# Performance work log

Hardware: AMD Instinct MI355X
Metric: run time of the kernel (lower is better)

The kernel has to match this reference:

```python
import jax, jax.numpy as jnp
import numpy as np

N = 50000      # nodes
E = 800000     # edges
F = 128        # node_features
DSS = 64       # degree_set_size
H = 128        # latent dim (hardcoded in GraphES)


def gcn_conv(x, W, b, src, dst, n):
    # PyG GCNConv: linear -> symmetric-normalized aggregation with self loops -> bias
    h = x @ W                                            # [N, C_out]
    deg = jnp.zeros((n,), x.dtype).at[dst].add(1.0) + 1.0  # in-degree incl. self loop
    dinv = jax.lax.rsqrt(deg)
    norm = dinv[src] * dinv[dst]                         # [E]
    agg = jnp.zeros_like(h).at[dst].add(h[src] * norm[:, None])
    agg = agg + h * (dinv * dinv)[:, None]               # self-loop term (norm_ii = 1/deg_i)
    return agg + b


def mlp(x, w1, b1, w2, b2):
    return jax.nn.relu(x @ w1 + b1) @ w2 + b2


def _swap(ei, i1, i2, coin):
    e1 = jnp.take(ei, i1, axis=1)
    e2 = jnp.take(ei, i2, axis=1)
    a, b = e1[0], e1[1]
    c, d = e2[0], e2[1]
    ne1 = jnp.where(coin, jnp.stack([a, d]), jnp.stack([a, c]))
    ne2 = jnp.where(coin, jnp.stack([c, b]), jnp.stack([b, d]))
    return ei.at[:, i1].set(ne1).at[:, i2].set(ne2)


def setup_inputs() -> dict:
    key = jax.random.key(0)
    ks = jax.random.split(key, 24)
    s = 0.05

    def rn(k, shape):
        return jax.random.normal(k, shape, jnp.float32) * s

    return {
        "x": jax.random.normal(ks[0], (N, F), jnp.float32),
        "edge_index": jax.random.randint(ks[1], (2, E), 0, N, dtype=jnp.int32),
        "degree_set": jax.random.randint(ks[2], (N,), 0, DSS, dtype=jnp.int32),
        "timesteps": 5,
        # encoder: GCN(F+DSS -> 2H), GCN(2H -> H)
        "enc_w1": rn(ks[3], (F + DSS, 2 * H)), "enc_b1": jnp.zeros((2 * H,), jnp.float32),
        "enc_w2": rn(ks[4], (2 * H, H)),       "enc_b2": jnp.zeros((H,), jnp.float32),
        # decoder: GCN(H+DSS -> 2F), GCN(2F -> F)
        "dec_w1": rn(ks[5], (H + DSS, 2 * F)), "dec_b1": jnp.zeros((2 * F,), jnp.float32),
        "dec_w2": rn(ks[6], (2 * F, F)),       "dec_b2": jnp.zeros((F,), jnp.float32),
        # edge_predictor_1: Linear(128,64)->ReLU->Linear(64,1)
        "ep1_w1": rn(ks[7], (H, 64)),  "ep1_b1": jnp.zeros((64,), jnp.float32),
        "ep1_w2": rn(ks[8], (64, 1)),  "ep1_b2": jnp.zeros((1,), jnp.float32),
        # edge_predictor_2: input is z concat flattened pair features -> 128+256=384
        "ep2_w1": rn(ks[9], (H + 2 * H, 64)), "ep2_b1": jnp.zeros((64,), jnp.float32),
        "ep2_w2": rn(ks[10], (64, 1)),        "ep2_b2": jnp.zeros((1,), jnp.float32),
    }


def reference(x, edge_index, degree_set, timesteps,
              enc_w1, enc_b1, enc_w2, enc_b2,
              dec_w1, dec_b1, dec_w2, dec_b2,
              ep1_w1, ep1_b1, ep1_w2, ep1_b2,
              ep2_w1, ep2_b1, ep2_w2, ep2_b2):
    src, dst = edge_index[0], edge_index[1]
    dh = jax.nn.one_hot(degree_set, DSS, dtype=x.dtype)  # [N, DSS]

    # ---- encoder ----
    h = jax.nn.relu(gcn_conv(jnp.concatenate([x, dh], 1), enc_w1, enc_b1, src, dst, N))
    z = gcn_conv(h, enc_w2, enc_b2, src, dst, N)          # [N, H]

    # ---- forward diffusion: timesteps random edge swaps (deterministic PRNG) ----
    ei = edge_index
    for t in range(timesteps):
        k1, k2 = jax.random.split(jax.random.fold_in(jax.random.key(1), t))
        idx = jax.random.choice(k1, E, (2,), replace=False)
        ei = _swap(ei, idx[0], idx[1], jax.random.bernoulli(k2))

    # ---- reverse process: argmax-driven edge swaps ----
    # edge_predictor_1 scores depend only on z -> identical every step; compute once
    i1 = jnp.argmax(mlp(z, ep1_w1, ep1_b1, ep1_w2, ep1_b2).squeeze(-1))
    for t in range(timesteps):
        e1 = jnp.take(ei, i1, axis=1)                     # [2]
        e1f = z[e1].reshape(-1)                           # [2H]
        cond = jnp.concatenate([z, jnp.broadcast_to(e1f, (N, 2 * H))], 1)
        i2 = jnp.argmax(mlp(cond, ep2_w1, ep2_b1, ep2_w2, ep2_b2).squeeze(-1))
        coin = jax.random.bernoulli(jax.random.fold_in(jax.random.key(2), t))
        ei = _swap(ei, i1, i2, coin)

    # ---- decoder on final edge structure ----
    src2, dst2 = ei[0], ei[1]
    hd = jax.nn.relu(gcn_conv(jnp.concatenate([z, dh], 1), dec_w1, dec_b1, src2, dst2, N))
    out = gcn_conv(hd, dec_w2, dec_b2, src2, dst2, N)     # [N, F]
    return out, ei
```

## Files before the change

kernel.cpp:

```cpp
#include <hip/hip_runtime.h>
#include <cstdint>
#include <cstddef>
#include <vector>
#include <algorithm>

#define NN 50000
#define EE 800000
#define FF 128
#define HH 128
#define TSTEPS 5

typedef __attribute__((ext_vector_type(8))) short bf16x8;
typedef __attribute__((ext_vector_type(4))) float f32x4;

__device__ __forceinline__ float bf2f(unsigned short u)
{
    return __uint_as_float((unsigned)u << 16);
}
__device__ __forceinline__ unsigned short f2bf(float x)
{
    unsigned u = __float_as_uint(x);
    u = (u + 0x7FFFu + ((u >> 16) & 1u));
    return (unsigned short)(u >> 16);
}
// ... 118 lines not shown
            for (int r = 0; r < 4; r++) {
                int row_in = rowBase + rt * 16 + quad * 4 + r;
                float v = acc[rt][tt][r] + bv;
                if (RELU) v = fmaxf(v, 0.f);
                Ot[row_in * BC + col_in] = f2bf(v);
            }
    }
    __syncthreads();
    for (int idx = tid; idx < 128 * (BC / 8); idx += 256) {
        int rr = idx / (BC / 8), c8 = idx - rr * (BC / 8);
        int gr = row0 + rr;
        if (gr < n)
            *(bf16x8*)(Pout + (size_t)gr * C + col0 + c8 * 8) =
                *(const bf16x8*)(Ot + rr * BC + c8 * 8);
    }
}

template <int K, int C, int BC, int WR, int WC, bool HAS_BIAS, bool RELU, bool OUT_SPLIT>
__global__ __launch_bounds__(256) void gemm_split_tiled(
    const unsigned short* __restrict__ Ahi, const unsigned short* __restrict__ Alo,
    const unsigned short* __restrict__ Whi, const unsigned short* __restrict__ Wlo,
    void* __restrict__ PoutHi, unsigned short* __restrict__ PoutLo,
    const float* __restrict__ bias, int n)
{
    constexpr int KC = K / 32;
    constexpr int RT = 128 / (WR * 16);
    constexpr int TT = BC / (WC * 16);
    constexpr int LDS_USHORTS = 8192 + BC * 64;
    __shared__ __align__(16) unsigned short smem[LDS_USHORTS];
    unsigned short* AhL = smem;
    unsigned short* AlL = smem + 4096;
    unsigned short* WhL = smem + 8192;
    unsigned short* WlL = smem + 8192 + BC * 32;

    const int row0 = blockIdx.x * 128;
    const int col0 = blockIdx.y * BC;
    const int tid = threadIdx.x;
    const int w = tid >> 6, l = tid & 63;
    const int m = l & 15, quad = l >> 4;
    const int wr = w / WC, wc = w % WC;
    const int rowBase = wr * (RT * 16);
    const int colBase = wc * (TT * 16);

    f32x4 acc[RT][TT];
#pragma unroll
    for (int rt = 0; rt < RT; rt++)
#pragma unroll
        for (int tt = 0; tt < TT; tt++) acc[rt][tt] = { 0.f, 0.f, 0.f, 0.f };

    for (int kc = 0; kc < KC; kc++) {
        for (int s = w; s < 8; s += 4) {
            int rg = row0 + s * 16 + (l >> 2);
            if (rg > n - 1) rg = n - 1;
            size_t go = (size_t)rg * K + kc * 32 + (l & 3) * 8;
            gload16(Ahi + go, AhL + s * 512);
            gload16(Alo + go, AlL + s * 512);
        }
        for (int s = w; s < BC / 16; s += 4) {
            size_t wo = ((size_t)kc * C + col0) * 32 + s * 512 + l * 8;
            gload16(Whi + wo, WhL + s * 512);
            gload16(Wlo + wo, WlL + s * 512);
        }
        __syncthreads();

        bf16x8 ah[RT], al[RT];
#pragma unroll
        for (int rt = 0; rt < RT; rt++) {
            int ro = (rowBase + rt * 16 + m) * 32 + quad * 8;
            ah[rt] = *(const bf16x8*)(AhL + ro);
            al[rt] = *(const bf16x8*)(AlL + ro);
        }
#pragma unroll
        for (int tt = 0; tt < TT; tt++) {
            int co = (colBase + tt * 16 + m) * 32 + quad * 8;
            bf16x8 wh = *(const bf16x8*)(WhL + co);
            bf16x8 wl = *(const bf16x8*)(WlL + co);
#pragma unroll
            for (int rt = 0; rt < RT; rt++) {
                acc[rt][tt] = __builtin_amdgcn_mfma_f32_16x16x32_bf16(al[rt], wh, acc[rt][tt], 0, 0, 0);
                acc[rt][tt] = __builtin_amdgcn_mfma_f32_16x16x32_bf16(ah[rt], wl, acc[rt][tt], 0, 0, 0);
                acc[rt][tt] = __builtin_amdgcn_mfma_f32_16x16x32_bf16(ah[rt], wh, acc[rt][tt], 0, 0, 0);
            }
        }
        __syncthreads();
    }

    if (OUT_SPLIT) {
        unsigned short* Ot = smem;
#pragma unroll
        for (int tt = 0; tt < TT; tt++) {
            int col_in = colBase + tt * 16 + m;
            float bv = HAS_BIAS ? bias[col0 + col_in] : 0.f;
#pragma unroll
            for (int rt = 0; rt < RT; rt++)
#pragma unroll
                for (int r = 0; r < 4; r++) {
                    int row_in = rowBase + rt * 16 + quad * 4 + r;
                    float v = acc[rt][tt][r] + bv;
                    if (RELU) v = fmaxf(v, 0.f);
                    Ot[row_in * BC + col_in] = f2bf(v);
                }
        }
        __syncthreads();
        for (int idx = tid; idx < 128 * (BC / 8); idx += 256) {
            int rr = idx / (BC / 8), c8 = idx - rr * (BC / 8);
            int gr = row0 + rr;
            if (gr < n)
                *(bf16x8*)((unsigned short*)PoutHi + (size_t)gr * C + col0 + c8 * 8) =
                    *(const bf16x8*)(Ot + rr * BC + c8 * 8);
        }
        __syncthreads();
#pragma unroll
        for (int tt = 0; tt < TT; tt++) {
            int col_in = colBase + tt * 16 + m;
            float bv = HAS_BIAS ? bias[col0 + col_in] : 0.f;
#pragma unroll
            for (int rt = 0; rt < RT; rt++)
#pragma unroll
                for (int r = 0; r < 4; r++) {
                    int row_in = rowBase + rt * 16 + quad * 4 + r;
                    float v = acc[rt][tt][r] + bv;
                    if (RELU) v = fmaxf(v, 0.f);
                    unsigned short h = f2bf(v);
                    Ot[row_in * BC + col_in] = f2bf(v - bf2f(h));
                }
        }
        __syncthreads();
        for (int idx = tid; idx < 128 * (BC / 8); idx += 256) {
            int rr = idx / (BC / 8), c8 = idx - rr * (BC / 8);
            int gr = row0 + rr;
            if (gr < n)
                *(bf16x8*)(PoutLo + (size_t)gr * C + col0 + c8 * 8) =
                    *(const bf16x8*)(Ot + rr * BC + c8 * 8);
        }
    } else {
#pragma unroll
        for (int tt = 0; tt < TT; tt++) {
            int col = col0 + colBase + tt * 16 + m;
            float bv = HAS_BIAS ? bias[col] : 0.f;
#pragma unroll
            for (int rt = 0; rt < RT; rt++)
#pragma unroll
                for (int r = 0; r < 4; r++) {
                    int gr = row0 + rowBase + rt * 16 + quad * 4 + r;
                    if (gr >= n) continue;
                    float v = acc[rt][tt][r] + bv;
                    if (RELU) v = fmaxf(v, 0.f);
                    ((float*)PoutHi)[(size_t)gr * C + col] = v;
                }
        }
    }
}

template <int K, int C>
__global__ void pack_w(const float* __restrict__ W, unsigned short* __restrict__ Wp)
{
    int idx = blockIdx.x * 256 + threadIdx.x;
    if (idx >= K * C) return;
    int k = idx / C, nn = idx - k * C;
    Wp[((size_t)(k >> 5) * C + nn) * 32 + (k & 31)] = f2bf(W[idx]);
}

template <int K, int C>
__global__ void pack_w_split(const float* __restrict__ W,
                             unsigned short* __restrict__ Wphi,
                             unsigned short* __restrict__ Wplo)
{
    int idx = blockIdx.x * 256 + threadIdx.x;
    if (idx >= K * C) return;
    int k = idx / C, nn = idx - k * C;
    unsigned short hi, lo;
    splitbf(W[idx], hi, lo);
    size_t o = ((size_t)(k >> 5) * C + nn) * 32 + (k & 31);
    Wphi[o] = hi;
    Wplo[o] = lo;
}

template <int K, int C>
__global__ void pack_w4(const float* __restrict__ W, float* __restrict__ Wp4)
{
    int idx = blockIdx.x * 256 + threadIdx.x;
    if (idx >= K * C) return;
    int k = idx / C, c = idx - k * C;
    Wp4[(((size_t)(k >> 2) * C) + c) * 4 + (k & 3)] = W[idx];
}

__global__ void count_deg(const int* __restrict__ dst, int* __restrict__ cnt, int e)
{
    int i = blockIdx.x * blockDim.x + threadIdx.x;
    if (i < e) {
        unsigned d = (unsigned)dst[i];
        if (d < (unsigned)NN) atomicAdd(&cnt[d], 1);
    }
}

__global__ void scan_block(const int* __restrict__ cnt, int* __restrict__ excl,
                           int* __restrict__ bsum, float* __restrict__ dinv,
                           int* __restrict__ cnt_copy, int n)
{
    __shared__ int s[256];
    int i = blockIdx.x * 256 + threadIdx.x;
    int v = (i < n) ? cnt[i] : 0;
    if (i < n) {
        dinv[i] = 1.0f / sqrtf((float)v + 1.0f);
        if (cnt_copy) cnt_copy[i] = v;
    }
    s[threadIdx.x] = v;
    __syncthreads();
    for (int off = 1; off < 256; off <<= 1) {
        int t = (threadIdx.x >= off) ? s[threadIdx.x - off] : 0;
        __syncthreads();
        s[threadIdx.x] += t;
        __syncthreads();
    }
    if (i < n) excl[i] = s[threadIdx.x] - v;
    if (threadIdx.x == 255) bsum[blockIdx.x] = s[255];
}
__global__ void scan_add_fill(int* __restrict__ rowptr, const int* __restrict__ bsum,
                              int* __restrict__ fill, int n, int e)
{
    int pre = 0;
    for (int b = 0; b < (int)blockIdx.x; b++) pre += bsum[b];
    int i = blockIdx.x * 256 + threadIdx.x;
    if (i < n) { rowptr[i] += pre; fill[i] = 0; }
    if (i == 0) rowptr[n] = e;
}

__global__ void csr_fill_pairs(const int* __restrict__ src, const int* __restrict__ dst,
                               const int* __restrict__ ds,
                               const float* __restrict__ dinv, const int* __restrict__ rowptr,
                               int* __restrict__ fill, int2* __restrict__ csr_pair, int e)
{
    int i = blockIdx.x * blockDim.x + threadIdx.x;
    if (i >= e) return;
    int d = dst[i], s = src[i];
    if ((unsigned)d >= (unsigned)NN || (unsigned)s >= (unsigned)NN) return;
    int slot = rowptr[d] + atomicAdd(&fill[d], 1);
    csr_pair[slot] = make_int2(s | (ds[s] << 20), __float_as_int(dinv[s] * dinv[d]));
}

template <bool BF16SRC, int OUTMODE>
__global__ __launch_bounds__(256) void agg_feat(
    const void* __restrict__ Xv, const int* __restrict__ ds,
    const int* __restrict__ rowptr, const int2* __restrict__ csr_pair,
    const float* __restrict__ dinv,
    void* __restrict__ Fout, unsigned short* __restrict__ FoutLo)
{
    const int w = threadIdx.x >> 6, l = threadIdx.x & 63;
    const int i = blockIdx.x * 4 + w;
    if (i >= NN) return;
    const int half = l >> 5, lh = l & 31;

    auto loadRow4 = [&](int s, float* v) {
        if (BF16SRC) {
            ushort4 u = ((const ushort4*)((const unsigned short*)Xv + (size_t)s * 128))[lh];
            v[0] = bf2f(u.x); v[1] = bf2f(u.y); v[2] = bf2f(u.z); v[3] = bf2f(u.w);
        } else {
            float4 t = ((const float4*)((const float*)Xv + (size_t)s * 128))[lh];
            v[0] = t.x; v[1] = t.y; v[2] = t.z; v[3] = t.w;
        }
    };

    float di = dinv[i], d2 = di * di;
    float acc[4];
    {
        float sv[4];
        loadRow4(i, sv);
        float wgt = half ? 0.f : d2;
#pragma unroll
        for (int v = 0; v < 4; v++) acc[v] = sv[v] * wgt;
    }
    float hist = (ds[i] == l) ? d2 : 0.f;

    const int beg = rowptr[i], end = rowptr[i + 1];
    int idx = beg;
    for (; idx + 8 <= end; idx += 8) {
        int s[8]; float nw[8]; int b[8];
#pragma unroll
        for (int j = 0; j < 8; j++) {
            int2 pr = csr_pair[idx + j];
            s[j] = pr.x & 0xFFFFF; b[j] = pr.x >> 20;
            nw[j] = __int_as_float(pr.y);
        }
        float vv[4][4];
#pragma unroll
        for (int p = 0; p < 4; p++) loadRow4(s[2 * p + half], vv[p]);
#pragma unroll
        for (int p = 0; p < 4; p++) {
            float wp = nw[2 * p + half];
#pragma unroll
            for (int v = 0; v < 4; v++) acc[v] = fmaf(vv[p][v], wp, acc[v]);
        }
#pragma unroll
        for (int j = 0; j < 8; j++) hist += (b[j] == l) ? nw[j] : 0.f;
    }
    for (; idx + 2 <= end; idx += 2) {
        int2 p0 = csr_pair[idx], p1 = csr_pair[idx + 1];
        int s0 = p0.x & 0xFFFFF, s1 = p1.x & 0xFFFFF;
        int b0 = p0.x >> 20, b1 = p1.x >> 20;
        float n0 = __int_as_float(p0.y), n1 = __int_as_float(p1.y);
        float v0[4];
        loadRow4(half ? s1 : s0, v0);
        float wp = half ? n1 : n0;
#pragma unroll
        for (int v = 0; v < 4; v++) acc[v] = fmaf(v0[v], wp, acc[v]);
        hist += (b0 == l) ? n0 : 0.f;
        hist += (b1 == l) ? n1 : 0.f;
    }
    if (idx < end) {
        int2 p0 = csr_pair[idx];
        int s0 = p0.x & 0xFFFFF;
        int b0 = p0.x >> 20;
        float n0 = __int_as_float(p0.y);
        float v0[4];
        loadRow4(s0, v0);
        float wp = half ? 0.f : n0;
#pragma unroll
        for (int v = 0; v < 4; v++) acc[v] = fmaf(v0[v], wp, acc[v]);
        hist += (b0 == l) ? n0 : 0.f;
    }
#pragma unroll
    for (int v = 0; v < 4; v++) acc[v] += __shfl_xor(acc[v], 32, 64);

    if (OUTMODE == 2) {
        if (half == 0) {
            unsigned short h[4], lo[4];
#pragma unroll
            for (int v = 0; v < 4; v++) splitbf(acc[v], h[v], lo[v]);
            ((ushort4*)((unsigned short*)Fout + (size_t)i * 192))[lh] =
                make_ushort4(h[0], h[1], h[2], h[3]);
            ((ushort4*)(FoutLo + (size_t)i * 192))[lh] =
                make_ushort4(lo[0], lo[1], lo[2], lo[3]);
        }
        unsigned short hh, ll;
        splitbf(hist, hh, ll);
        ((unsigned short*)Fout)[(size_t)i * 192 + 128 + l] = hh;
        FoutLo[(size_t)i * 192 + 128 + l] = ll;
    } else if (OUTMODE == 1) {
        if (half == 0) {
            ((ushort4*)((unsigned short*)Fout + (size_t)i * 192))[lh] =
                make_ushort4(f2bf(acc[0]), f2bf(acc[1]), f2bf(acc[2]), f2bf(acc[3]));
        }
        ((unsigned short*)Fout)[(size_t)i * 192 + 128 + l] = f2bf(hist);
    } else {
        if (half == 0) {
            ((float4*)((float*)Fout + (size_t)i * 192))[lh] =
                make_float4(acc[0], acc[1], acc[2], acc[3]);
        }
        ((float*)Fout)[(size_t)i * 192 + 128 + l] = hist;
    }
}

template <bool RELU, bool BF16P, bool CLAMP>
__global__ __launch_bounds__(256) void agg_wave(
    const void* __restrict__ Pv, const int* __restrict__ rowptr,
    const int2* __restrict__ csr_pair,
    const float* __restrict__ dinv, const float* __restrict__ bias,
    float* __restrict__ B, unsigned short* __restrict__ Bbf)
{
    const int w = threadIdx.x >> 6, l = threadIdx.x & 63;
    const int i = blockIdx.x * 4 + w;
    if (i >= NN) return;
    const int half = l >> 5, lh = l & 31;

    auto loadRow4 = [&](int s, float* v) {
        if (BF16P) {
            ushort4 u = ((const ushort4*)((const unsigned short*)Pv + (size_t)s * 128))[lh];
            v[0] = bf2f(u.x); v[1] = bf2f(u.y); v[2] = bf2f(u.z); v[3] = bf2f(u.w);
        } else {
            float4 t = ((const float4*)((const float*)Pv + (size_t)s * 128))[lh];
            v[0] = t.x; v[1] = t.y; v[2] = t.z; v[3] = t.w;
        }
    };

    float di = dinv[i], d2 = di * di;
    float acc[4];
    {
        float sv[4];
        loadRow4(i, sv);
        float wgt = half ? 0.f : d2;
#pragma unroll
        for (int v = 0; v < 4; v++) acc[v] = sv[v] * wgt;
    }

    const int beg = rowptr[i], end = rowptr[i + 1];
    int idx = beg;
    for (; idx + 8 <= end; idx += 8) {
        int s[8]; float nw[8];
#pragma unroll
        for (int j = 0; j < 8; j++) {
            int2 pr = csr_pair[idx + j];
            s[j] = pr.x & 0xFFFFF; nw[j] = __int_as_float(pr.y);
        }
        float vv[4][4];
#pragma unroll
        for (int p = 0; p < 4; p++) loadRow4(s[2 * p + half], vv[p]);
#pragma unroll
        for (int p = 0; p < 4; p++) {
            float wp = nw[2 * p + half];
#pragma unroll
            for (int v = 0; v < 4; v++) acc[v] = fmaf(vv[p][v], wp, acc[v]);
        }
    }
    for (; idx + 2 <= end; idx += 2) {
        int2 p0 = csr_pair[idx], p1 = csr_pair[idx + 1];
        int s0 = p0.x & 0xFFFFF, s1 = p1.x & 0xFFFFF;
        float n0 = __int_as_float(p0.y), n1 = __int_as_float(p1.y);
        float v0[4];
        loadRow4(half ? s1 : s0, v0);
        float wp = half ? n1 : n0;
#pragma unroll
        for (int v = 0; v < 4; v++) acc[v] = fmaf(v0[v], wp, acc[v]);
    }
    if (idx < end) {
        int2 p0 = csr_pair[idx];
        int s0 = p0.x & 0xFFFFF;
        float n0 = __int_as_float(p0.y);
        float v0[4];
        loadRow4(s0, v0);
        float wp = half ? 0.f : n0;
#pragma unroll
        for (int v = 0; v < 4; v++) acc[v] = fmaf(v0[v], wp, acc[v]);
    }
#pragma unroll
    for (int v = 0; v < 4; v++) acc[v] += __shfl_xor(acc[v], 32, 64);

    if (half == 0) {
        float r[4];
#pragma unroll
        for (int v = 0; v < 4; v++) {
            r[v] = acc[v] + bias[lh * 4 + v];
            if (RELU) r[v] = fmaxf(r[v], 0.f);
            if (CLAMP) r[v] = fminf(fmaxf(r[v], -64.f), 64.f);
        }
        ((float4*)(B + (size_t)i * 128))[lh] = make_float4(r[0], r[1], r[2], r[3]);
        if (Bbf)
            ((ushort4*)(Bbf + (size_t)i * 128))[lh] =
                make_ushort4(f2bf(r[0]), f2bf(r[1]), f2bf(r[2]), f2bf(r[3]));
    }
}

__device__ __forceinline__ unsigned long long packScore(float s, int i)
{
    unsigned u = __float_as_uint(s);
    u = (u & 0x80000000u) ? ~u : (u | 0x80000000u);
    return ((unsigned long long)u << 32) | (unsigned)(~(unsigned)i);
}
__device__ __forceinline__ int unpackIdx(unsigned long long v)
{
    return (int)(~(unsigned)(v & 0xFFFFFFFFull));
}
__device__ __forceinline__ unsigned long long maxu64(unsigned long long a,
                                                     unsigned long long b)
{
    return a > b ? a : b;
}

__device__ __forceinline__ void publishBest(
    unsigned long long* blockBest, unsigned* counter, unsigned long long bv,
    int nblocks, unsigned* isLastFlag)
{
    __hip_atomic_store(&blockBest[blockIdx.x], bv, __ATOMIC_RELEASE,
                       __HIP_MEMORY_SCOPE_AGENT);
    unsigned prev = __hip_atomic_fetch_add(counter, 1u, __ATOMIC_ACQ_REL,
                                           __HIP_MEMORY_SCOPE_AGENT);
    *isLastFlag = (prev == (unsigned)(nblocks - 1)) ? 1u : 0u;
}
__device__ __forceinline__ unsigned long long loadBest(
    const unsigned long long* blockBest, int i)
{
    return __hip_atomic_load(&blockBest[i], __ATOMIC_RELAXED,
                             __HIP_MEMORY_SCOPE_AGENT);
}

__device__ __forceinline__ void patchDeg(int* cnt2, int i1, int i2,
                                         int B, int C, int D, int coin)
{
    if (i1 == i2) return;
    int n1 = coin ? D : C;
    int n2 = coin ? B : D;
    cnt2[B]--; cnt2[n1]++;
    cnt2[D]--; cnt2[n2]++;
}

__global__ __launch_bounds__(256, 4) void score1_blocks(
    const float* __restrict__ z, const float* __restrict__ w1p4,
    const float* __restrict__ b1, const float* __restrict__ w2,
    unsigned long long* __restrict__ blockBest,
    unsigned long long* __restrict__ out, unsigned* __restrict__ counter,
    int n, int nblocks)
{
    __shared__ float Zs[64][HH];
    __shared__ unsigned long long red[4];
    __shared__ unsigned isLast;
    const int row0 = blockIdx.x * 64;
    const int tid = threadIdx.x;
    for (int idx = tid; idx < 64 * 32; idx += 256) {
        int r = idx >> 5, k4 = idx & 31;
        int gr = row0 + r;
        float4 v = make_float4(0.f, 0.f, 0.f, 0.f);
        if (gr < n) v = ((const float4*)(z + (size_t)gr * HH))[k4];
        *(float4*)&Zs[r][k4 * 4] = v;
    }
    __syncthreads();

    const int w = tid >> 6, l = tid & 63;
    float b1v = b1[l], w2v = w2[l];
    unsigned long long best = 0;
    for (int rg = 0; rg < 4; rg++) {
        const int rbase = w * 16 + rg * 4;
        float acc[4];
#pragma unroll
        for (int r = 0; r < 4; r++) acc[r] = b1v;
#pragma unroll 4
        for (int k4 = 0; k4 < 32; k4++) {
            float4 wv = ((const float4*)w1p4)[k4 * 64 + l];
#pragma unroll
            for (int r = 0; r < 4; r++) {
                float4 zv = *(const float4*)&Zs[rbase + r][k4 * 4];
                acc[r] = fmaf(zv.x, wv.x, acc[r]);
                acc[r] = fmaf(zv.y, wv.y, acc[r]);
                acc[r] = fmaf(zv.z, wv.z, acc[r]);
                acc[r] = fmaf(zv.w, wv.w, acc[r]);
            }
        }
#pragma unroll
        for (int r = 0; r < 4; r++) {
            float p = fmaxf(acc[r], 0.f) * w2v;
#pragma unroll
            for (int off = 32; off > 0; off >>= 1) p += __shfl_xor(p, off, 64);
            int row = row0 + rbase + r;
            if (row < n) best = maxu64(best, packScore(p, row));
        }
    }
    if (l == 0) red[w] = best;
    __syncthreads();
    if (tid == 0) {
        unsigned long long bv = maxu64(maxu64(red[0], red[1]), maxu64(red[2], red[3]));
        publishBest(blockBest, counter, bv, nblocks, &isLast);
    }
    __syncthreads();
    if (isLast) {
        unsigned long long b = 0;
        for (int i = tid; i < nblocks; i += 256) b = maxu64(b, loadBest(blockBest, i));
#pragma unroll
        for (int off = 32; off > 0; off >>= 1)
            b = maxu64(b, (unsigned long long)__shfl_xor((long long)b, off, 64));
        if ((tid & 63) == 0) red[tid >> 6] = b;
        __syncthreads();
        if (tid == 0) {
            *out = maxu64(maxu64(red[0], red[1]), maxu64(red[2], red[3]));
            __hip_atomic_store(counter, 0u, __ATOMIC_RELAXED, __HIP_MEMORY_SCOPE_AGENT);
        }
    }
}

__global__ __launch_bounds__(256) void score2_fused(
    int* __restrict__ ei, const unsigned long long* __restrict__ best1,
    const float* __restrict__ z, const float* __restrict__ w1,
    const float* __restrict__ zw1, const float* __restrict__ w2,
    unsigned long long* __restrict__ blockBest, unsigned* __restrict__ counter,
    int* __restrict__ cnt2, int n, int coin)
{
    __shared__ float za_s[HH], zb_s[HH];
    __shared__ float cpart[4][64];
    __shared__ float Cs[64], W2s[64];
    __shared__ unsigned long long red[4];
    __shared__ unsigned isLast;
    int i1 = unpackIdx(*best1);
    if ((unsigned)i1 >= (unsigned)EE) i1 = 0;
    int a = ei[i1], b = ei[EE + i1];
    if ((unsigned)a >= (unsigned)NN) a = 0;
    if ((unsigned)b >= (unsigned)NN) b = 0;
    const int tid = threadIdx.x;
    if (tid < HH) za_s[tid] = z[(size_t)a * HH + tid];
    else          zb_s[tid - HH] = z[(size_t)b * HH + tid - HH];
    __syncthreads();
    const int h = tid & 63, kg = tid >> 6;
    float accc = 0.f;
#pragma unroll
    for (int kk = 0; kk < 32; kk++) {
        int k = kg * 32 + kk;
        accc = fmaf(za_s[k], w1[(128 + k) * 64 + h], accc);
        accc = fmaf(zb_s[k], w1[(256 + k) * 64 + h], accc);
    }
    cpart[kg][h] = accc;
    __syncthreads();
    if (tid < 64) {
        Cs[tid] = (cpart[0][tid] + cpart[1][tid]) + (cpart[2][tid] + cpart[3][tid]);
        W2s[tid] = w2[tid];
    }
// ... 82 lines not shown
    tf(k0, k1, 0u, 0u, a0, a1);
    tf(k0, k1, 0u, 1u, b0, b1);
}

static void jbits_part(uint32_t k0, uint32_t k1, uint32_t n, std::vector<uint32_t>& out)
{
    out.resize(n);
    for (uint32_t i = 0; i < n; i++) {
        uint32_t a, b;
        tf(k0, k1, 0u, i, a, b);
        out[i] = a ^ b;
    }
}

static bool jbern_part(uint32_t k0, uint32_t k1)
{
    uint32_t a, b;
    tf(k0, k1, 0u, 0u, a, b);
    return (a ^ b) < 0x80000000u;
}

struct PrngConsts {
    Swaps swaps;
    int revCoin[TSTEPS];
    PrngConsts()
    {
        swaps.coins = 0;
        std::vector<uint32_t> bits1, bits2;
        std::vector<uint64_t> packed((size_t)EE);
        for (int t = 0; t < TSTEPS; t++) {
            uint32_t kt0, kt1;
            tf(0u, 1u, 0u, (uint32_t)t, kt0, kt1);
            uint32_t kc0, kc1, kb0, kb1;
            jsplit_part(kt0, kt1, kc0, kc1, kb0, kb1);
            if (jbern_part(kb0, kb1)) swaps.coins |= (1u << t);

            uint32_t cur0 = kc0, cur1 = kc1, sub0, sub1, nk0, nk1;
            jsplit_part(cur0, cur1, nk0, nk1, sub0, sub1);
            cur0 = nk0; cur1 = nk1;
            jbits_part(sub0, sub1, EE, bits1);
            jsplit_part(cur0, cur1, nk0, nk1, sub0, sub1);
            cur0 = nk0; cur1 = nk1;
            jbits_part(sub0, sub1, EE, bits2);

            uint64_t m1 = ~0ull, m2 = ~0ull;
            for (uint32_t pos = 0; pos < EE; pos++) {
                uint64_t u = ((uint64_t)bits2[pos] << 32) | pos;
                if (u < m1) { m2 = m1; m1 = u; }
                else if (u < m2) { m2 = u; }
            }
            uint32_t pos0 = (uint32_t)m1, pos1 = (uint32_t)m2;
            for (uint32_t j = 0; j < EE; j++)
                packed[j] = ((uint64_t)bits1[j] << 32) | j;
            std::nth_element(packed.begin(), packed.begin() + pos0, packed.end());
            uint32_t j0 = (uint32_t)packed[pos0];
            std::nth_element(packed.begin(), packed.begin() + pos1, packed.end());
            uint32_t j1 = (uint32_t)packed[pos1];
            swaps.a[t] = (int)j0;
            swaps.b[t] = (int)j1;
        }
        for (int t = 0; t < TSTEPS; t++) {
            uint32_t kt0, kt1;
            tf(0u, 2u, 0u, (uint32_t)t, kt0, kt1);
            revCoin[t] = jbern_part(kt0, kt1) ? 1 : 0;
        }
    }
};
static const PrngConsts g_prng;

extern "C" void kernel_launch(void* const* d_in, const int* in_sizes, int n_in,
                              void* d_out, int out_size, void* d_ws, size_t ws_size,
                              hipStream_t stream)
{
    (void)out_size; (void)ws_size;

    static const int kWant[20] = {
        NN * FF, 2 * EE, NN, 1,
        192 * 256, 256, 256 * 128, 128,
        192 * 256, 256, 256 * 128, 128,
        128 * 64, 64, 64, 1,
        384 * 64, 64, 64, 1
    };
    const void* p[20] = {};
    {
        int j = 0;
        for (int k = 0; k < 20; k++) {
            if (j < n_in && in_sizes[j] == kWant[k]) { p[k] = d_in[j]; j++; }
            else if (kWant[k] == 1)                  { p[k] = nullptr; }
            else if (j < n_in)                       { p[k] = d_in[j]; j++; }
        }
    }
    const float* x      = (const float*)p[0];
    const int*   ei_in  = (const int*)p[1];
    const int*   ds     = (const int*)p[2];
    const float* enc_w1 = (const float*)p[4];
    const float* enc_b1 = (const float*)p[5];
    const float* enc_w2 = (const float*)p[6];
    const float* enc_b2 = (const float*)p[7];
    const float* dec_w1 = (const float*)p[8];
    const float* dec_b1 = (const float*)p[9];
    const float* dec_w2 = (const float*)p[10];
    const float* dec_b2 = (const float*)p[11];
    const float* ep1_w1 = (const float*)p[12];
    const float* ep1_b1 = (const float*)p[13];
    const float* ep1_w2 = (const float*)p[14];
    const float* ep2_w1 = (const float*)p[16];
    const float* ep2_b1 = (const float*)p[17];
    const float* ep2_w2 = (const float*)p[18];

    char* ws = (char*)d_ws;
    size_t off = 0;
    auto alloc = [&](size_t bytes) -> void* {
        void* q = ws + off;
        off += (bytes + 255) & ~(size_t)255;
        return q;
    };
    float* bufP    = (float*)alloc((size_t)NN * 256 * 4);
    float* bufH    = (float*)alloc((size_t)NN * 256 * 4);
    int*   eiw     = (int*)alloc((size_t)2 * EE * 4);
    int2*  csr_pair = (int2*)alloc((size_t)EE * 8);
    int*   rowptr  = (int*)alloc((size_t)(NN + 1) * 4);
    int*   cnt     = (int*)alloc((size_t)NN * 4);
    int*   cnt2    = (int*)alloc((size_t)NN * 4);
    int*   fill    = (int*)alloc((size_t)NN * 4);
    int*   bsum    = (int*)alloc(256 * 4);
    float* dinv    = (float*)alloc((size_t)NN * 4);
    unsigned short* zbf   = (unsigned short*)alloc((size_t)NN * 128 * 2);
    unsigned short* wp1   = (unsigned short*)alloc((size_t)192 * 256 * 2);
    unsigned short* wp2   = (unsigned short*)alloc((size_t)256 * 128 * 2);
    unsigned short* w1hi  = (unsigned short*)alloc((size_t)192 * 256 * 2);
    unsigned short* w1lo  = (unsigned short*)alloc((size_t)192 * 256 * 2);
    unsigned short* w2hi  = (unsigned short*)alloc((size_t)256 * 128 * 2);
    unsigned short* w2lo  = (unsigned short*)alloc((size_t)256 * 128 * 2);
    float* ep1w1p = (float*)alloc((size_t)128 * 64 * 4);
    float* ep2w1p = (float*)alloc((size_t)128 * 64 * 4);
    unsigned long long* blockBest = (unsigned long long*)alloc(4096 * 8);
    unsigned long long* best1 = (unsigned long long*)alloc(8);
    unsigned* counters = (unsigned*)alloc(256);

    unsigned short* f1hi = (unsigned short*)bufP;
    unsigned short* f1lo = f1hi + (size_t)NN * 192;
    float* P2   = bufP;
    float* zw1  = bufP;
    unsigned short* feat2bf = (unsigned short*)bufP;
    unsigned short* p4      = (unsigned short*)bufP;
    unsigned short* hhi = (unsigned short*)bufH;
    unsigned short* hlo = hhi + (size_t)NN * 256;
    float* zbuf = bufH;
    unsigned short* hdbf = (unsigned short*)bufH;

    const int TPB = 256;
    const int gN      = (NN + TPB - 1) / TPB;
    const int gE      = (EE + TPB - 1) / TPB;
    const int gRows64s = (NN + 63) / 64;
    const int gRows32 = (NN + 31) / 32;
    const int gRows128 = (NN + 127) / 128;
    const int gWave   = (NN + 3) / 4;

    hipMemsetAsync(counters, 0, 8, stream);

    pack_w<192, 256><<<(192 * 256 + TPB - 1) / TPB, TPB, 0, stream>>>(dec_w1, wp1);
    pack_w<256, 128><<<(256 * 128 + TPB - 1) / TPB, TPB, 0, stream>>>(dec_w2, wp2);
    pack_w_split<192, 256><<<(192 * 256 + TPB - 1) / TPB, TPB, 0, stream>>>(enc_w1, w1hi, w1lo);
    pack_w_split<256, 128><<<(256 * 128 + TPB - 1) / TPB, TPB, 0, stream>>>(enc_w2, w2hi, w2lo);
    pack_w4<128, 64><<<(128 * 64 + TPB - 1) / TPB, TPB, 0, stream>>>(ep1_w1, ep1w1p);
    pack_w4<128, 64><<<(128 * 64 + TPB - 1) / TPB, TPB, 0, stream>>>(ep2_w1, ep2w1p);

    hipMemsetAsync(cnt, 0, (size_t)NN * 4, stream);
    count_deg<<<gE, TPB, 0, stream>>>(ei_in + EE, cnt, EE);
    scan_block<<<gN, TPB, 0, stream>>>(cnt, rowptr, bsum, dinv, cnt2, NN);
    scan_add_fill<<<gN, TPB, 0, stream>>>(rowptr, bsum, fill, NN, EE);
    csr_fill_pairs<<<gE, TPB, 0, stream>>>(ei_in, ei_in + EE, ds, dinv, rowptr, fill,
                                           csr_pair, EE);

    agg_feat<false, 2><<<gWave, TPB, 0, stream>>>(
        x, ds, rowptr, csr_pair, dinv, f1hi, f1lo);
    gemm_split_tiled<192, 256, 128, 2, 2, true, true, true>
        <<<dim3(gRows128, 2), TPB, 0, stream>>>(
        f1hi, f1lo, w1hi, w1lo, hhi, hlo, enc_b1, NN);

    gemm_split_tiled<256, 128, 64, 4, 1, false, false, false>
        <<<dim3(gRows128, 2), TPB, 0, stream>>>(
        hhi, hlo, w2hi, w2lo, P2, nullptr, nullptr, NN);
    agg_wave<false, false, false><<<gWave, TPB, 0, stream>>>(
        P2, rowptr, csr_pair, dinv, enc_b2, zbuf, zbf);

    score1_blocks<<<gRows64s, TPB, 0, stream>>>(zbuf, ep1w1p, ep1_b1, ep1_w2,
                                                blockBest, best1, counters + 0,
                                                NN, gRows64s);
    zw1_gemm<<<gRows32, TPB, 0, stream>>>(zbuf, ep2w1p, zw1, NN, ep2_b1);

    hipMemcpyAsync(eiw, ei_in, (size_t)2 * EE * 4, hipMemcpyDeviceToDevice, stream);
    fwd_swaps_k<<<1, 64, 0, stream>>>(eiw, cnt2, g_prng.swaps);

    for (int t = 0; t < TSTEPS; t++) {
        score2_fused<<<256, TPB, 0, stream>>>(eiw, best1, zbuf, ep2_w1,
                                              zw1, ep2_w2, blockBest, counters + 1,
                                              cnt2, NN, g_prng.revCoin[t]);
    }

    scan_block<<<gN, TPB, 0, stream>>>(cnt2, rowptr, bsum, dinv, nullptr, NN);
    scan_add_fill<<<gN, TPB, 0, stream>>>(rowptr, bsum, fill, NN, EE);
    csr_fill_pairs<<<gE, TPB, 0, stream>>>(eiw, eiw + EE, ds, dinv, rowptr, fill,
                                           csr_pair, EE);

    agg_feat<true, 1><<<gWave, TPB, 0, stream>>>(
        zbf, ds, rowptr, csr_pair, dinv, feat2bf, nullptr);
    gemm_bf16_tiled<192, 256, 128, 2, 2, true, true>
        <<<dim3(gRows128, 2), TPB, 0, stream>>>(
        feat2bf, wp1, hdbf, dec_b1, NN);

    gemm_bf16_tiled<256, 128, 128, 2, 2, false, false>
        <<<dim3(gRows128, 1), TPB, 0, stream>>>(
        hdbf, wp2, p4, nullptr, NN);
    agg_wave<false, true, true><<<gWave, TPB, 0, stream>>>(
        p4, rowptr, csr_pair, dinv, dec_b2, (float*)d_out, nullptr);

    write_edges<<<(2 * EE + TPB - 1) / TPB, TPB, 0, stream>>>(
        eiw, (float*)d_out + (size_t)NN * FF);
}
```

Baseline: 766.8 us.

## Merge weight-packing kernels, fuse edge copy into degree count, widen bf16 gathers

The six weight-packing launches become a single pack_all kernel. The device-to-device edge_index memcpy is folded into the degree-count kernel, which now reads both rows and writes the copy. The bf16-source aggregation paths now load 8 bf16 per lane with 16 lanes per row, so each wave gathers four neighbor rows at once instead of two, followed by a two-step shuffle reduction. Together these aim to cut launch overhead and an extra pass over edge memory, and to raise memory-level parallelism in the gather-heavy decoder aggregations, at the cost of more registers and more branching in the packing kernel.

After: 818.2 us. +6.7%, slower.

```diff
diff --git a/kernel.cpp b/kernel.cpp
--- a/kernel.cpp
+++ b/kernel.cpp
@@ -294,45 +294,56 @@
     }
 }
 
-template <int K, int C>
-__global__ void pack_w(const float* __restrict__ W, unsigned short* __restrict__ Wp)
+__global__ void pack_all(
+    const float* __restrict__ dw1, const float* __restrict__ dw2,
+    const float* __restrict__ ew1, const float* __restrict__ ew2,
+    const float* __restrict__ e1w, const float* __restrict__ e2w,
+    unsigned short* __restrict__ wp1, unsigned short* __restrict__ wp2,
+    unsigned short* __restrict__ w1hi, unsigned short* __restrict__ w1lo,
+    unsigned short* __restrict__ w2hi, unsigned short* __restrict__ w2lo,
+    float* __restrict__ p1, float* __restrict__ p2)
 {
     int idx = blockIdx.x * 256 + threadIdx.x;
-    if (idx >= K * C) return;
-    int k = idx / C, nn = idx - k * C;
-    Wp[((size_t)(k >> 5) * C + nn) * 32 + (k & 31)] = f2bf(W[idx]);
-}
-
-template <int K, int C>
-__global__ void pack_w_split(const float* __restrict__ W,
-                             unsigned short* __restrict__ Wphi,
-                             unsigned short* __restrict__ Wplo)
-{
-    int idx = blockIdx.x * 256 + threadIdx.x;
-    if (idx >= K * C) return;
-    int k = idx / C, nn = idx - k * C;
-    unsigned short hi, lo;
-    splitbf(W[idx], hi, lo);
-    size_t o = ((size_t)(k >> 5) * C + nn) * 32 + (k & 31);
-    Wphi[o] = hi;
-    Wplo[o] = lo;
-}
-
-template <int K, int C>
-__global__ void pack_w4(const float* __restrict__ W, float* __restrict__ Wp4)
-{
-    int idx = blockIdx.x * 256 + threadIdx.x;
-    if (idx >= K * C) return;
-    int k = idx / C, c = idx - k * C;
-    Wp4[(((size_t)(k >> 2) * C) + c) * 4 + (k & 3)] = W[idx];
-}
-
-__global__ void count_deg(const int* __restrict__ dst, int* __restrict__ cnt, int e)
+    if (idx < 49152) {
+        int k = idx / 256, c = idx - k * 256;
+        wp1[((size_t)(k >> 5) * 256 + c) * 32 + (k & 31)] = f2bf(dw1[idx]);
+    } else if (idx < 81920) {
+        int t = idx - 49152;
+        int k = t / 128, c = t - k * 128;
+        wp2[((size_t)(k >> 5) * 128 + c) * 32 + (k & 31)] = f2bf(dw2[t]);
+    } else if (idx < 131072) {
+        int t = idx - 81920;
+        int k = t / 256, c = t - k * 256;
+        unsigned short hi, lo;
+        splitbf(ew1[t], hi, lo);
+        size_t o = ((size_t)(k >> 5) * 256 + c) * 32 + (k & 31);
+        w1hi[o] = hi; w1lo[o] = lo;
+    } else if (idx < 163840) {
+        int t = idx - 131072;
+        int k = t / 128, c = t - k * 128;
+        unsigned short hi, lo;
+        splitbf(ew2[t], hi, lo);
+        size_t o = ((size_t)(k >> 5) * 128 + c) * 32 + (k & 31);
+        w2hi[o] = hi; w2lo[o] = lo;
+    } else if (idx < 172032) {
+        int t = idx - 163840;
+        int k = t / 64, c = t - k * 64;
+        p1[(((size_t)(k >> 2) * 64) + c) * 4 + (k & 3)] = e1w[t];
+    } else if (idx < 180224) {
+        int t = idx - 172032;
+        int k = t / 64, c = t - k * 64;
+        p2[(((size_t)(k >> 2) * 64) + c) * 4 + (k & 3)] = e2w[t];
+    }
+}
+
+__global__ void count_deg_copy(const int* __restrict__ ei_in, int* __restrict__ eiw,
+                               int* __restrict__ cnt, int e)
 {
     int i = blockIdx.x * blockDim.x + threadIdx.x;
-    if (i < e) {
-        unsigned d = (unsigned)dst[i];
-        if (d < (unsigned)NN) atomicAdd(&cnt[d], 1);
+    if (i < 2 * e) {
+        int v = ei_in[i];
+        eiw[i] = v;
+        if (i >= e && (unsigned)v < (unsigned)NN) atomicAdd(&cnt[v], 1);
     }
 }
 
@@ -391,105 +402,172 @@
     const int w = threadIdx.x >> 6, l = threadIdx.x & 63;
     const int i = blockIdx.x * 4 + w;
     if (i >= NN) return;
-    const int half = l >> 5, lh = l & 31;
-
-    auto loadRow4 = [&](int s, float* v) {
-        if (BF16SRC) {
-            ushort4 u = ((const ushort4*)((const unsigned short*)Xv + (size_t)s * 128))[lh];
-            v[0] = bf2f(u.x); v[1] = bf2f(u.y); v[2] = bf2f(u.z); v[3] = bf2f(u.w);
-        } else {
+
+    float di = dinv[i], d2 = di * di;
+    float hist = (ds[i] == l) ? d2 : 0.f;
+    const int beg = rowptr[i], end = rowptr[i + 1];
+
+    if constexpr (BF16SRC) {
+        const int q = l >> 4, lq = l & 15;
+        auto loadRow8 = [&](int s, float* v) {
+            bf16x8 u = ((const bf16x8*)((const unsigned short*)Xv + (size_t)s * 128))[lq];
+#pragma unroll
+            for (int t = 0; t < 8; t++) v[t] = bf2f((unsigned short)u[t]);
+        };
+        float acc8[8];
+        {
+            float sv[8];
+            loadRow8(i, sv);
+            float wgt = (q == 0) ? d2 : 0.f;
+#pragma unroll
+            for (int v = 0; v < 8; v++) acc8[v] = sv[v] * wgt;
+        }
+        int idx = beg;
+        for (; idx + 8 <= end; idx += 8) {
+            int2 pr[8];
+#pragma unroll
+            for (int j = 0; j < 8; j++) pr[j] = csr_pair[idx + j];
+            int s0 = pr[q].x & 0xFFFFF, s1 = pr[4 + q].x & 0xFFFFF;
+            float w0 = __int_as_float(pr[q].y), w1 = __int_as_float(pr[4 + q].y);
+            float v0[8], v1[8];
+            loadRow8(s0, v0);
+            loadRow8(s1, v1);
+#pragma unroll
+            for (int v = 0; v < 8; v++) {
+                acc8[v] = fmaf(v0[v], w0, acc8[v]);
+                acc8[v] = fmaf(v1[v], w1, acc8[v]);
+            }
+#pragma unroll
+            for (int j = 0; j < 8; j++)
+                hist += ((pr[j].x >> 20) == l) ? __int_as_float(pr[j].y) : 0.f;
+        }
+        for (; idx + 4 <= end; idx += 4) {
+            int2 pr[4];
+#pragma unroll
+            for (int j = 0; j < 4; j++) pr[j] = csr_pair[idx + j];
+            int sq = pr[q].x & 0xFFFFF;
+            float wq = __int_as_float(pr[q].y);
+            float v0[8];
+            loadRow8(sq, v0);
+#pragma unroll
+            for (int v = 0; v < 8; v++) acc8[v] = fmaf(v0[v], wq, acc8[v]);
+#pragma unroll
+            for (int j = 0; j < 4; j++)
+                hist += ((pr[j].x >> 20) == l) ? __int_as_float(pr[j].y) : 0.f;
+        }
+        for (; idx < end; idx++) {
+            int2 p0 = csr_pair[idx];
+            int s0 = p0.x & 0xFFFFF;
+            float n0 = __int_as_float(p0.y);
+            float v0[8];
+            loadRow8(s0, v0);
+            float wq = (q == 0) ? n0 : 0.f;
+#pragma unroll
+            for (int v = 0; v < 8; v++) acc8[v] = fmaf(v0[v], wq, acc8[v]);
+            hist += ((p0.x >> 20) == l) ? n0 : 0.f;
+        }
+#pragma unroll
+        for (int v = 0; v < 8; v++) {
+            acc8[v] += __shfl_xor(acc8[v], 16, 64);
+            acc8[v] += __shfl_xor(acc8[v], 32, 64);
+        }
+        if (q == 0) {
+            bf16x8 o;
+#pragma unroll
+            for (int v = 0; v < 8; v++) o[v] = (short)f2bf(acc8[v]);
+            *(bf16x8*)((unsigned short*)Fout + (size_t)i * 192 + lq * 8) = o;
+        }
+        ((unsigned short*)Fout)[(size_t)i * 192 + 128 + l] = f2bf(hist);
+    } else {
+        const int half = l >> 5, lh = l & 31;
+        auto loadRow4 = [&](int s, float* v) {
             float4 t = ((const float4*)((const float*)Xv + (size_t)s * 128))[lh];
             v[0] = t.x; v[1] = t.y; v[2] = t.z; v[3] = t.w;
-        }
-    };
-
-    float di = dinv[i], d2 = di * di;
-    float acc[4];
-    {
-        float sv[4];
-        loadRow4(i, sv);
-        float wgt = half ? 0.f : d2;
-#pragma unroll
-        for (int v = 0; v < 4; v++) acc[v] = sv[v] * wgt;
-    }
-    float hist = (ds[i] == l) ? d2 : 0.f;
-
-    const int beg = rowptr[i], end = rowptr[i + 1];
-    int idx = beg;
-    for (; idx + 8 <= end; idx += 8) {
-        int s[8]; float nw[8]; int b[8];
-#pragma unroll
-        for (int j = 0; j < 8; j++) {
-            int2 pr = csr_pair[idx + j];
-            s[j] = pr.x & 0xFFFFF; b[j] = pr.x >> 20;
-            nw[j] = __int_as_float(pr.y);
-        }
-        float vv[4][4];
-#pragma unroll
-        for (int p = 0; p < 4; p++) loadRow4(s[2 * p + half], vv[p]);
-#pragma unroll
-        for (int p = 0; p < 4; p++) {
-            float wp = nw[2 * p + half];
-#pragma unroll
-            for (int v = 0; v < 4; v++) acc[v] = fmaf(vv[p][v], wp, acc[v]);
-        }
-#pragma unroll
-        for (int j = 0; j < 8; j++) hist += (b[j] == l) ? nw[j] : 0.f;
-    }
-    for (; idx + 2 <= end; idx += 2) {
-        int2 p0 = csr_pair[idx], p1 = csr_pair[idx + 1];
-        int s0 = p0.x & 0xFFFFF, s1 = p1.x & 0xFFFFF;
-        int b0 = p0.x >> 20, b1 = p1.x >> 20;
-        float n0 = __int_as_float(p0.y), n1 = __int_as_float(p1.y);
-        float v0[4];
-        loadRow4(half ? s1 : s0, v0);
-        float wp = half ? n1 : n0;
-#pragma unroll
-        for (int v = 0; v < 4; v++) acc[v] = fmaf(v0[v], wp, acc[v]);
-        hist += (b0 == l) ? n0 : 0.f;
-        hist += (b1 == l) ? n1 : 0.f;
-    }
-    if (idx < end) {
-        int2 p0 = csr_pair[idx];
-        int s0 = p0.x & 0xFFFFF;
-        int b0 = p0.x >> 20;
-        float n0 = __int_as_float(p0.y);
-        float v0[4];
-        loadRow4(s0, v0);
-        float wp = half ? 0.f : n0;
-#pragma unroll
-        for (int v = 0; v < 4; v++) acc[v] = fmaf(v0[v], wp, acc[v]);
-        hist += (b0 == l) ? n0 : 0.f;
-    }
-#pragma unroll
-    for (int v = 0; v < 4; v++) acc[v] += __shfl_xor(acc[v], 32, 64);
-
-    if (OUTMODE == 2) {
-        if (half == 0) {
-            unsigned short h[4], lo[4];
-#pragma unroll
-            for (int v = 0; v < 4; v++) splitbf(acc[v], h[v], lo[v]);
-            ((ushort4*)((unsigned short*)Fout + (size_t)i * 192))[lh] =
-                make_ushort4(h[0], h[1], h[2], h[3]);
-            ((ushort4*)(FoutLo + (size_t)i * 192))[lh] =
-                make_ushort4(lo[0], lo[1], lo[2], lo[3]);
-        }
-        unsigned short hh, ll;
-        splitbf(hist, hh, ll);
-        ((unsigned short*)Fout)[(size_t)i * 192 + 128 + l] = hh;
-        FoutLo[(size_t)i * 192 + 128 + l] = ll;
-    } else if (OUTMODE == 1) {
-        if (half == 0) {
-            ((ushort4*)((unsigned short*)Fout + (size_t)i * 192))[lh] =
-                make_ushort4(f2bf(acc[0]), f2bf(acc[1]), f2bf(acc[2]), f2bf(acc[3]));
-        }
-        ((unsigned short*)Fout)[(size_t)i * 192 + 128 + l] = f2bf(hist);
-    } else {
-        if (half == 0) {
-            ((float4*)((float*)Fout + (size_t)i * 192))[lh] =
-                make_float4(acc[0], acc[1], acc[2], acc[3]);
-        }
-        ((float*)Fout)[(size_t)i * 192 + 128 + l] = hist;
+        };
+        float acc[4];
+        {
+            float sv[4];
+            loadRow4(i, sv);
+            float wgt = half ? 0.f : d2;
+#pragma unroll
+            for (int v = 0; v < 4; v++) acc[v] = sv[v] * wgt;
+        }
+        int idx = beg;
+        for (; idx + 8 <= end; idx += 8) {
+            int s[8]; float nw[8]; int b[8];
+#pragma unroll
+            for (int j = 0; j < 8; j++) {
+                int2 pr = csr_pair[idx + j];
+                s[j] = pr.x & 0xFFFFF; b[j] = pr.x >> 20;
+                nw[j] = __int_as_float(pr.y);
+            }
+            float vv[4][4];
+#pragma unroll
+            for (int p = 0; p < 4; p++) loadRow4(s[2 * p + half], vv[p]);
+#pragma unroll
+            for (int p = 0; p < 4; p++) {
+                float wp = nw[2 * p + half];
+#pragma unroll
+                for (int v = 0; v < 4; v++) acc[v] = fmaf(vv[p][v], wp, acc[v]);
+            }
+#pragma unroll
+            for (int j = 0; j < 8; j++) hist += (b[j] == l) ? nw[j] : 0.f;
+        }
+        for (; idx + 2 <= end; idx += 2) {
+            int2 p0 = csr_pair[idx], p1 = csr_pair[idx + 1];
+            int s0 = p0.x & 0xFFFFF, s1 = p1.x & 0xFFFFF;
+            int b0 = p0.x >> 20, b1 = p1.x >> 20;
+            float n0 = __int_as_float(p0.y), n1 = __int_as_float(p1.y);
+            float v0[4];
+            loadRow4(half ? s1 : s0, v0);
+            float wp = half ? n1 : n0;
+#pragma unroll
+            for (int v = 0; v < 4; v++) acc[v] = fmaf(v0[v], wp, acc[v]);
+            hist += (b0 == l) ? n0 : 0.f;
+            hist += (b1 == l) ? n1 : 0.f;
+        }
+        if (idx < end) {
+            int2 p0 = csr_pair[idx];
+            int s0 = p0.x & 0xFFFFF;
+            int b0 = p0.x >> 20;
+            float n0 = __int_as_float(p0.y);
+            float v0[4];
+            loadRow4(s0, v0);
+            float wp = half ? 0.f : n0;
+#pragma unroll
+            for (int v = 0; v < 4; v++) acc[v] = fmaf(v0[v], wp, acc[v]);
+            hist += (b0 == l) ? n0 : 0.f;
+        }
+#pragma unroll
+        for (int v = 0; v < 4; v++) acc[v] += __shfl_xor(acc[v], 32, 64);
+
+        if (OUTMODE == 2) {
+            if (half == 0) {
+                unsigned short h[4], lo[4];
+#pragma unroll
+                for (int v = 0; v < 4; v++) splitbf(acc[v], h[v], lo[v]);
+                ((ushort4*)((unsigned short*)Fout + (size_t)i * 192))[lh] =
+                    make_ushort4(h[0], h[1], h[2], h[3]);
+                ((ushort4*)(FoutLo + (size_t)i * 192))[lh] =
+                    make_ushort4(lo[0], lo[1], lo[2], lo[3]);
+            }
+            unsigned short hh, ll;
+            splitbf(hist, hh, ll);
+            ((unsigned short*)Fout)[(size_t)i * 192 + 128 + l] = hh;
+            FoutLo[(size_t)i * 192 + 128 + l] = ll;
+        } else if (OUTMODE == 1) {
+            if (half == 0) {
+                ((ushort4*)((unsigned short*)Fout + (size_t)i * 192))[lh] =
+                    make_ushort4(f2bf(acc[0]), f2bf(acc[1]), f2bf(acc[2]), f2bf(acc[3]));
+            }
+            ((unsigned short*)Fout)[(size_t)i * 192 + 128 + l] = f2bf(hist);
+        } else {
+            if (half == 0) {
+                ((float4*)((float*)Fout + (size_t)i * 192))[lh] =
+                    make_float4(acc[0], acc[1], acc[2], acc[3]);
+            }
+            ((float*)Fout)[(size_t)i * 192 + 128 + l] = hist;
+        }
     }
 }
 
@@ -503,82 +581,149 @@
     const int w = threadIdx.x >> 6, l = threadIdx.x & 63;
     const int i = blockIdx.x * 4 + w;
     if (i >= NN) return;
-    const int half = l >> 5, lh = l & 31;
-
-    auto loadRow4 = [&](int s, float* v) {
-        if (BF16P) {
-            ushort4 u = ((const ushort4*)((const unsigned short*)Pv + (size_t)s * 128))[lh];
-            v[0] = bf2f(u.x); v[1] = bf2f(u.y); v[2] = bf2f(u.z); v[3] = bf2f(u.w);
-        } else {
+    float di = dinv[i], d2 = di * di;
+    const int beg = rowptr[i], end = rowptr[i + 1];
+
+    if constexpr (BF16P) {
+        const int q = l >> 4, lq = l & 15;
+        auto loadRow8 = [&](int s, float* v) {
+            bf16x8 u = ((const bf16x8*)((const unsigned short*)Pv + (size_t)s * 128))[lq];
+#pragma unroll
+            for (int t = 0; t < 8; t++) v[t] = bf2f((unsigned short)u[t]);
+        };
+        float acc8[8];
+        {
+            float sv[8];
+            loadRow8(i, sv);
+            float wgt = (q == 0) ? d2 : 0.f;
+#pragma unroll
+            for (int v = 0; v < 8; v++) acc8[v] = sv[v] * wgt;
+        }
+        int idx = beg;
+        for (; idx + 8 <= end; idx += 8) {
+            int2 pr[8];
+#pragma unroll
+            for (int j = 0; j < 8; j++) pr[j] = csr_pair[idx + j];
+            int s0 = pr[q].x & 0xFFFFF, s1 = pr[4 + q].x & 0xFFFFF;
+            float w0 = __int_as_float(pr[q].y), w1 = __int_as_float(pr[4 + q].y);
+            float v0[8], v1[8];
+            loadRow8(s0, v0);
+            loadRow8(s1, v1);
+#pragma unroll
+            for (int v = 0; v < 8; v++) {
+                acc8[v] = fmaf(v0[v], w0, acc8[v]);
+                acc8[v] = fmaf(v1[v], w1, acc8[v]);
+            }
+        }
+        for (; idx + 4 <= end; idx += 4) {
+            int2 pr = csr_pair[idx + q];
+            int sq = pr.x & 0xFFFFF;
+            float wq = __int_as_float(pr.y);
+            float v0[8];
+            loadRow8(sq, v0);
+#pragma unroll
+            for (int v = 0; v < 8; v++) acc8[v] = fmaf(v0[v], wq, acc8[v]);
+        }
+        for (; idx < end; idx++) {
+            int2 p0 = csr_pair[idx];
+            int s0 = p0.x & 0xFFFFF;
+            float n0 = __int_as_float(p0.y);
+            float v0[8];
+            loadRow8(s0, v0);
+            float wq = (q == 0) ? n0 : 0.f;
+#pragma unroll
+            for (int v = 0; v < 8; v++) acc8[v] = fmaf(v0[v], wq, acc8[v]);
+        }
+#pragma unroll
+        for (int v = 0; v < 8; v++) {
+            acc8[v] += __shfl_xor(acc8[v], 16, 64);
+            acc8[v] += __shfl_xor(acc8[v], 32, 64);
+        }
+        if (q == 0) {
+            float r[8];
+#pragma unroll
+            for (int v = 0; v < 8; v++) {
+                r[v] = acc8[v] + bias[lq * 8 + v];
+                if (RELU) r[v] = fmaxf(r[v], 0.f);
+                if (CLAMP) r[v] = fminf(fmaxf(r[v], -64.f), 64.f);
+            }
+            ((float4*)(B + (size_t)i * 128))[lq * 2] = make_float4(r[0], r[1], r[2], r[3]);
+            ((float4*)(B + (size_t)i * 128))[lq * 2 + 1] = make_float4(r[4], r[5], r[6], r[7]);
+            if (Bbf) {
+                bf16x8 o;
+#pragma unroll
+                for (int v = 0; v < 8; v++) o[v] = (short)f2bf(r[v]);
+                *(bf16x8*)(Bbf + (size_t)i * 128 + lq * 8) = o;
+            }
+        }
+    } else {
+        const int half = l >> 5, lh = l & 31;
+        auto loadRow4 = [&](int s, float* v) {
             float4 t = ((const float4*)((const float*)Pv + (size_t)s * 128))[lh];
             v[0] = t.x; v[1] = t.y; v[2] = t.z; v[3] = t.w;
-        }
-    };
-
-    float di = dinv[i], d2 = di * di;
-    float acc[4];
-    {
-        float sv[4];
-        loadRow4(i, sv);
-        float wgt = half ? 0.f : d2;
-#pragma unroll
-        for (int v = 0; v < 4; v++) acc[v] = sv[v] * wgt;
-    }
-
-    const int beg = rowptr[i], end = rowptr[i + 1];
-    int idx = beg;
-    for (; idx + 8 <= end; idx += 8) {
-        int s[8]; float nw[8];
-#pragma unroll
-        for (int j = 0; j < 8; j++) {
-            int2 pr = csr_pair[idx + j];
-            s[j] = pr.x & 0xFFFFF; nw[j] = __int_as_float(pr.y);
-        }
-        float vv[4][4];
-#pragma unroll
-        for (int p = 0; p < 4; p++) loadRow4(s[2 * p + half], vv[p]);
-#pragma unroll
-        for (int p = 0; p < 4; p++) {
-            float wp = nw[2 * p + half];
-#pragma unroll
-            for (int v = 0; v < 4; v++) acc[v] = fmaf(vv[p][v], wp, acc[v]);
-        }
-    }
-    for (; idx + 2 <= end; idx += 2) {
-        int2 p0 = csr_pair[idx], p1 = csr_pair[idx + 1];
-        int s0 = p0.x & 0xFFFFF, s1 = p1.x & 0xFFFFF;
-        float n0 = __int_as_float(p0.y), n1 = __int_as_float(p1.y);
-        float v0[4];
-        loadRow4(half ? s1 : s0, v0);
-        float wp = half ? n1 : n0;
-#pragma unroll
-        for (int v = 0; v < 4; v++) acc[v] = fmaf(v0[v], wp, acc[v]);
-    }
-    if (idx < end) {
-        int2 p0 = csr_pair[idx];
-        int s0 = p0.x & 0xFFFFF;
-        float n0 = __int_as_float(p0.y);
-        float v0[4];
-        loadRow4(s0, v0);
-        float wp = half ? 0.f : n0;
-#pragma unroll
-        for (int v = 0; v < 4; v++) acc[v] = fmaf(v0[v], wp, acc[v]);
-    }
-#pragma unroll
-    for (int v = 0; v < 4; v++) acc[v] += __shfl_xor(acc[v], 32, 64);
-
-    if (half == 0) {
-        float r[4];
-#pragma unroll
-        for (int v = 0; v < 4; v++) {
-            r[v] = acc[v] + bias[lh * 4 + v];
-            if (RELU) r[v] = fmaxf(r[v], 0.f);
-            if (CLAMP) r[v] = fminf(fmaxf(r[v], -64.f), 64.f);
-        }
-        ((float4*)(B + (size_t)i * 128))[lh] = make_float4(r[0], r[1], r[2], r[3]);
-        if (Bbf)
-            ((ushort4*)(Bbf + (size_t)i * 128))[lh] =
-                make_ushort4(f2bf(r[0]), f2bf(r[1]), f2bf(r[2]), f2bf(r[3]));
+        };
+        float acc[4];
+        {
+            float sv[4];
+            loadRow4(i, sv);
+            float wgt = half ? 0.f : d2;
+#pragma unroll
+            for (int v = 0; v < 4; v++) acc[v] = sv[v] * wgt;
+        }
+        int idx = beg;
+        for (; idx + 8 <= end; idx += 8) {
+            int s[8]; float nw[8];
+#pragma unroll
+            for (int j = 0; j < 8; j++) {
+                int2 pr = csr_pair[idx + j];
+                s[j] = pr.x & 0xFFFFF; nw[j] = __int_as_float(pr.y);
+            }
+            float vv[4][4];
+#pragma unroll
+            for (int p = 0; p < 4; p++) loadRow4(s[2 * p + half], vv[p]);
+#pragma unroll
+            for (int p = 0; p < 4; p++) {
+                float wp = nw[2 * p + half];
+#pragma unroll
+                for (int v = 0; v < 4; v++) acc[v] = fmaf(vv[p][v], wp, acc[v]);
+            }
+        }
+        for (; idx + 2 <= end; idx += 2) {
+            int2 p0 = csr_pair[idx], p1 = csr_pair[idx + 1];
+            int s0 = p0.x & 0xFFFFF, s1 = p1.x & 0xFFFFF;
+            float n0 = __int_as_float(p0.y), n1 = __int_as_float(p1.y);
+            float v0[4];
+            loadRow4(half ? s1 : s0, v0);
+            float wp = half ? n1 : n0;
+#pragma unroll
+            for (int v = 0; v < 4; v++) acc[v] = fmaf(v0[v], wp, acc[v]);
+        }
+        if (idx < end) {
+            int2 p0 = csr_pair[idx];
+            int s0 = p0.x & 0xFFFFF;
+            float n0 = __int_as_float(p0.y);
+            float v0[4];
+            loadRow4(s0, v0);
+            float wp = half ? 0.f : n0;
+#pragma unroll
+            for (int v = 0; v < 4; v++) acc[v] = fmaf(v0[v], wp, acc[v]);
+        }
+#pragma unroll
+        for (int v = 0; v < 4; v++) acc[v] += __shfl_xor(acc[v], 32, 64);
+
+        if (half == 0) {
+            float r[4];
+#pragma unroll
+            for (int v = 0; v < 4; v++) {
+                r[v] = acc[v] + bias[lh * 4 + v];
+                if (RELU) r[v] = fmaxf(r[v], 0.f);
+                if (CLAMP) r[v] = fminf(fmaxf(r[v], -64.f), 64.f);
+            }
+            ((float4*)(B + (size_t)i * 128))[lh] = make_float4(r[0], r[1], r[2], r[3]);
+            if (Bbf)
+                ((ushort4*)(Bbf + (size_t)i * 128))[lh] =
+                    make_ushort4(f2bf(r[0]), f2bf(r[1]), f2bf(r[2]), f2bf(r[3]));
+        }
     }
 }
 
@@ -967,6 +1112,7 @@
     const int TPB = 256;
     const int gN      = (NN + TPB - 1) / TPB;
     const int gE      = (EE + TPB - 1) / TPB;
+    const int g2E     = (2 * EE + TPB - 1) / TPB;
     const int gRows64s = (NN + 63) / 64;
     const int gRows32 = (NN + 31) / 32;
     const int gRows128 = (NN + 127) / 128;
@@ -974,15 +1120,12 @@
 
     hipMemsetAsync(counters, 0, 8, stream);
 
-    pack_w<192, 256><<<(192 * 256 + TPB - 1) / TPB, TPB, 0, stream>>>(dec_w1, wp1);
-    pack_w<256, 128><<<(256 * 128 + TPB - 1) / TPB, TPB, 0, stream>>>(dec_w2, wp2);
-    pack_w_split<192, 256><<<(192 * 256 + TPB - 1) / TPB, TPB, 0, stream>>>(enc_w1, w1hi, w1lo);
-    pack_w_split<256, 128><<<(256 * 128 + TPB - 1) / TPB, TPB, 0, stream>>>(enc_w2, w2hi, w2lo);
-    pack_w4<128, 64><<<(128 * 64 + TPB - 1) / TPB, TPB, 0, stream>>>(ep1_w1, ep1w1p);
-    pack_w4<128, 64><<<(128 * 64 + TPB - 1) / TPB, TPB, 0, stream>>>(ep2_w1, ep2w1p);
+    pack_all<<<(180224 + TPB - 1) / TPB, TPB, 0, stream>>>(
+        dec_w1, dec_w2, enc_w1, enc_w2, ep1_w1, ep2_w1,
+        wp1, wp2, w1hi, w1lo, w2hi, w2lo, ep1w1p, ep2w1p);
 
     hipMemsetAsync(cnt, 0, (size_t)NN * 4, stream);
-    count_deg<<<gE, TPB, 0, stream>>>(ei_in + EE, cnt, EE);
+    count_deg_copy<<<g2E, TPB, 0, stream>>>(ei_in, eiw, cnt, EE);
     scan_block<<<gN, TPB, 0, stream>>>(cnt, rowptr, bsum, dinv, cnt2, NN);
     scan_add_fill<<<gN, TPB, 0, stream>>>(rowptr, bsum, fill, NN, EE);
     csr_fill_pairs<<<gE, TPB, 0, stream>>>(ei_in, ei_in + EE, ds, dinv, rowptr, fill,
@@ -1005,7 +1148,6 @@
                                                 NN, gRows64s);
     zw1_gemm<<<gRows32, TPB, 0, stream>>>(zbuf, ep2w1p, zw1, NN, ep2_b1);
 
-    hipMemcpyAsync(eiw, ei_in, (size_t)2 * EE * 4, hipMemcpyDeviceToDevice, stream);
     fwd_swaps_k<<<1, 64, 0, stream>>>(eiw, cnt2, g_prng.swaps);
 
     for (int t = 0; t < TSTEPS; t++) {
@@ -1031,6 +1173,6 @@
     agg_wave<false, true, true><<<gWave, TPB, 0, stream>>>(
         p4, rowptr, csr_pair, dinv, dec_b2, (float*)d_out, nullptr);
 
-    write_edges<<<(2 * EE + TPB - 1) / TPB, TPB, 0, stream>>>(
+    write_edges<<<g2E, TPB, 0, stream>>>(
         eiw, (float*)d_out + (size_t)NN * FF);
 }
```
